# Performance work log

Measured on AMD Instinct MI355X. Metric: run time of the kernel, lower is better.

Reference implementation:

```python
import jax, jax.numpy as jnp
import numpy as np

B, N, E, D, F_IN, EDGE_DIM, VN = 128, 500, 1048576, 128, 5, 2, 10
NEG_FEAT = 0.01   # torch F.leaky_relu default
NEG_ATT = 0.2     # GAT attention slope


def _gat_layer(h_in, src, dst, edge_attr, W, b, a_src, a_dst, a_edge, We, n_nodes):
    # Edge-feature GAT conv: per-edge attention over (src, dst, edge) then
    # softmax-normalized scatter-aggregate onto destination nodes.
    h = h_in @ W                                  # [N, d]
    e = edge_attr @ We                            # [E, d] projected edge features
    logits = jax.nn.leaky_relu((h @ a_src)[src] + (h @ a_dst)[dst] + e @ a_edge,
                               negative_slope=NEG_ATT)    # [E]
    # segment softmax over incoming edges of each dst node
    m = jax.ops.segment_max(logits, dst, num_segments=n_nodes)
    ex = jnp.exp(logits - m[dst])
    denom = jax.ops.segment_sum(ex, dst, num_segments=n_nodes)
    alpha = ex / (denom[dst] + 1e-16)             # [E]
    msg = h[src] + e                              # [E, d]
    out = jax.ops.segment_sum(alpha[:, None] * msg, dst, num_segments=n_nodes)
    return out + b


def setup_inputs() -> dict:
    key = jax.random.key(0)
    ks = jax.random.split(key, 20)
    s = 0.05
    return {
        'x': jax.random.normal(ks[0], (B * N, F_IN), jnp.float32),
        'edge_index': jax.random.randint(ks[1], (2, E), 0, B * N, jnp.int64 if jax.config.jax_enable_x64 else jnp.int32).astype(jnp.int32),
        'edge_attr': jax.random.uniform(ks[2], (E, EDGE_DIM), jnp.float32),
        'curr_v_node_id': jax.random.randint(ks[3], (B,), 0, VN).astype(jnp.int32),
        'v_graph_embedding': jax.random.normal(ks[4], (B, D), jnp.float32),
        'v_node_dense_embeddings': jax.random.normal(ks[5], (B, VN, D), jnp.float32),
        'p_W': jax.random.normal(ks[6], (F_IN, D), jnp.float32) * s,
        'p_b': jnp.zeros((D,), jnp.float32),
        'Ws': jax.random.normal(ks[7], (4, D, D), jnp.float32) * s,
        'bs': jnp.zeros((4, D), jnp.float32),
        'a_srcs': jax.random.normal(ks[8], (4, D), jnp.float32) * s,
        'a_dsts': jax.random.normal(ks[9], (4, D), jnp.float32) * s,
        'a_edges': jax.random.normal(ks[10], (4, D), jnp.float32) * s,
        'Wes': jax.random.normal(ks[11], (4, EDGE_DIM, D), jnp.float32) * s,
        'W5': jax.random.normal(ks[12], (D, 1), jnp.float32) * s,
        'b5': jnp.zeros((1,), jnp.float32),
        'a_src5': jax.random.normal(ks[13], (1,), jnp.float32) * s,
        'a_dst5': jax.random.normal(ks[14], (1,), jnp.float32) * s,
        'a_edge5': jax.random.normal(ks[15], (1,), jnp.float32) * s,
        'We5': jax.random.normal(ks[16], (EDGE_DIM, 1), jnp.float32) * s,
    }


def reference(x, edge_index, edge_attr, curr_v_node_id, v_graph_embedding,
              v_node_dense_embeddings, p_W, p_b, Ws, bs, a_srcs, a_dsts,
              a_edges, Wes, W5, b5, a_src5, a_dst5, a_edge5, We5):
    n_nodes = x.shape[0]
    src, dst = edge_index[0], edge_index[1]
    # gather current v-node embedding: [B, D]
    curr_emb = v_node_dense_embeddings[jnp.arange(B), curr_v_node_id]
    # linear + leaky_relu then broadcast-add of graph/node context
    h = jax.nn.leaky_relu(x @ p_W + p_b, negative_slope=NEG_FEAT)  # [B*N, D]
    h = h.reshape(B, N, D) + v_graph_embedding[:, None, :] + curr_emb[:, None, :]
    h = h.reshape(B * N, D)
    # 4 hidden edge-feature GAT layers (128 -> 128) with leaky_relu
    for l in range(4):
        h = _gat_layer(h, src, dst, edge_attr, Ws[l], bs[l], a_srcs[l],
                       a_dsts[l], a_edges[l], Wes[l], n_nodes)
        h = jax.nn.leaky_relu(h, negative_slope=NEG_FEAT)
    # output layer (128 -> 1), no activation
    h = _gat_layer(h, src, dst, edge_attr, W5, b5, a_src5, a_dst5, a_edge5,
                   We5, n_nodes)                    # [B*N, 1]
    return h.reshape(B, N)
```

## Files before the change

kernel.cpp:

```cpp
#include <hip/hip_runtime.h>
#include <hip/hip_bf16.h>

#define BB   128
#define NN   500
#define NV   64000
#define EE   1048576
#define DD   128
#define FIN  5
#define VNN  10
#define NBUK 250
#define BCAP 8192

typedef unsigned int   uint32;
typedef unsigned short u16b;
typedef __attribute__((ext_vector_type(8))) short short8;
typedef __attribute__((ext_vector_type(4))) float float4v;

#define P_ASRC  0
#define P_ADST  512
#define P_WE    1024
#define P_BIAS  2048
#define P_W5    2560
#define P_CVEC  2688
#define P_SC5   2700
#define P_TOT   2816

static __device__ __forceinline__ float bf2f(__hip_bfloat16 v) { return __bfloat162float(v); }
static __device__ __forceinline__ float lo2f(uint32 u) { return __uint_as_float(u << 16); }
static __device__ __forceinline__ float hi2f(uint32 u) { return __uint_as_float(u & 0xFFFF0000u); }
static __device__ __forceinline__ uint32 f2bf_bits(float f) {
    uint32 u = __float_as_uint(f);
    return (u + 0x7FFFu + ((u >> 16) & 1u)) >> 16;
}
static __device__ __forceinline__ uint32 pack2(float a, float b) {
    return (f2bf_bits(a) & 0xFFFFu) | (f2bf_bits(b) << 16);
}
static __device__ __forceinline__ float ldf(const void* p, int i, int flag) {
    return flag ? ((const float*)p)[i] : bf2f(((const __hip_bfloat16*)p)[i]);
}

__global__ void sniff_kernel(const unsigned short* __restrict__ p16, int* __restrict__ FLAG) {
    __shared__ int sHigh, sZero;
    if (threadIdx.x == 0) { sHigh = 0; sZero = 0; }
    __syncthreads();
    unsigned short v = p16[2 * threadIdx.x];
    if (v >= 0x8000u) atomicOr(&sHigh, 1);
    if (v == 0)       atomicAdd(&sZero, 1);
    __syncthreads();
    if (threadIdx.x == 0) FLAG[0] = (sHigh || sZero >= 128) ? 1 : 0;
}

__global__ void zero_out_kernel(void* __restrict__ out, const int* __restrict__ FLAG, float tag) {
    int i = blockIdx.x * blockDim.x + threadIdx.x;
    if (i >= NV) return;
    float v = (i == 0) ? tag : 0.f;
    if (FLAG[0]) ((float*)out)[i] = v;
    else         ((u16b*)out)[i] = (u16b)f2bf_bits(v);
}

__global__ void prep_kernel(const void* __restrict__ Wes, const void* __restrict__ aeg,
                            const void* __restrict__ We5, const void* __restrict__ ae5,
                            const void* __restrict__ asr, const void* __restrict__ ads,
                            const void* __restrict__ bs, const void* __restrict__ W5,
                            const void* __restrict__ b5, const void* __restrict__ as5,
                            const void* __restrict__ ad5, const int* __restrict__ FLAG,
                            float* __restrict__ PAR) {
    const int flag = FLAG[0];
    if (blockIdx.x == 0) {
        for (int i = threadIdx.x; i < 512; i += 256) PAR[P_ASRC + i] = ldf(asr, i, flag);
    } else if (blockIdx.x == 1) {
        for (int i = threadIdx.x; i < 512; i += 256) PAR[P_ADST + i] = ldf(ads, i, flag);
    } else if (blockIdx.x == 2) {
        for (int i = threadIdx.x; i < 1024; i += 256) PAR[P_WE + i] = ldf(Wes, i, flag);
    } else if (blockIdx.x == 3) {
        for (int i = threadIdx.x; i < 512; i += 256) PAR[P_BIAS + i] = ldf(bs, i, flag);
    } else if (blockIdx.x == 4) {
        int tid = threadIdx.x;
        if (tid < 128) {
            PAR[P_W5 + tid] = ldf(W5, tid, flag);
        } else if (tid < 136) {
            int l = (tid - 128) >> 1, r = (tid - 128) & 1;
            float s = 0.f;
            for (int ch = 0; ch < DD; ++ch)
                s += ldf(Wes, l * 256 + r * DD + ch, flag) * ldf(aeg, l * DD + ch, flag);
            PAR[P_CVEC + l * 2 + r] = s;
        } else if (tid == 136) {
            float ae = ldf(ae5, 0, flag);
            float w0 = ldf(We5, 0, flag), w1 = ldf(We5, 1, flag);
            PAR[P_CVEC + 8] = w0 * ae; PAR[P_CVEC + 9] = w1 * ae;
            PAR[P_CVEC + 10] = w0;     PAR[P_CVEC + 11] = w1;
            PAR[P_SC5 + 0] = ldf(b5, 0, flag);
            PAR[P_SC5 + 1] = ldf(as5, 0, flag);
            PAR[P_SC5 + 2] = ldf(ad5, 0, flag);
        }
    }
}

__global__ __launch_bounds__(256) void prepack_kernel(const void* __restrict__ Ws,
                                                      const int* __restrict__ FLAG,
                                                      u16b* __restrict__ WB) {
    const int flag = FLAG[0];
    int t = blockIdx.x * 256 + threadIdx.x;
    int lane = t & 63;
    int frag = t >> 6;
    int nchunk = frag & 7, kblk = (frag >> 3) & 3, l = frag >> 5;
    int n = nchunk * 16 + (lane & 15);
    int kbase = kblk * 32 + (lane >> 4) * 8;
#pragma unroll
    for (int j = 0; j < 8; ++j) {
        int idx = l * 16384 + (kbase + j) * 128 + n;
        u16b bits = flag ? (u16b)f2bf_bits(((const float*)Ws)[idx])
                         : ((const u16b*)Ws)[idx];
        WB[(size_t)t * 8 + j] = bits;
    }
}

__global__ __launch_bounds__(256) void proj_kernel(
        const void* __restrict__ x, const void* __restrict__ pW,
        const void* __restrict__ pb, const int* __restrict__ curr,
        const void* __restrict__ vge, const void* __restrict__ vnd,
        const int* __restrict__ FLAG, uint32* __restrict__ H) {
    const int flag = FLAG[0];
    const int n = blockIdx.x * 4 + (threadIdx.x >> 6);
    const int lane = threadIdx.x & 63;
    const int b = n / NN;
    int cv = curr[b]; if ((unsigned)cv >= VNN) cv = 0;
    float xv[FIN];
#pragma unroll
    for (int k = 0; k < FIN; ++k) xv[k] = ldf(x, n * FIN + k, flag);
    const int ch = lane * 2;
    float s0 = ldf(pb, ch, flag), s1 = ldf(pb, ch + 1, flag);
#pragma unroll
    for (int k = 0; k < FIN; ++k) {
        s0 = fmaf(xv[k], ldf(pW, k * DD + ch, flag), s0);
        s1 = fmaf(xv[k], ldf(pW, k * DD + ch + 1, flag), s1);
    }
    s0 = (s0 > 0.f) ? s0 : 0.01f * s0;
    s1 = (s1 > 0.f) ? s1 : 0.01f * s1;
    s0 += ldf(vge, b * DD + ch, flag) + ldf(vnd, (b * VNN + cv) * DD + ch, flag);
    s1 += ldf(vge, b * DD + ch + 1, flag) + ldf(vnd, (b * VNN + cv) * DD + ch + 1, flag);
    H[(size_t)n * 64 + lane] = pack2(s0, s1);
}

__global__ void init_kernel(int* __restrict__ gcur, int* __restrict__ counts) {
    int t = blockIdx.x * 256 + threadIdx.x;
    if (t < NBUK) gcur[t] = t * BCAP;
    if (t < 512) counts[NV + t] = 0;
}

__global__ __launch_bounds__(256) void bucketize_kernel(
        const int* __restrict__ src, const int* __restrict__ dst,
        const void* __restrict__ eaP, const int* __restrict__ FLAG,
        int* __restrict__ gcur, uint32* __restrict__ bukx, uint32* __restrict__ buky) {
    __shared__ int cnt[256];
    __shared__ int cur[256];
    const int flag = FLAG[0];
    const int t = threadIdx.x;
    const int e0 = blockIdx.x * 4096;
    cnt[t] = 0;
    __syncthreads();
    int d[16];
#pragma unroll
    for (int i = 0; i < 16; ++i) {
        d[i] = dst[e0 + i * 256 + t];
        if ((unsigned)d[i] >= NV) d[i] = -1;
        if (d[i] >= 0) atomicAdd(&cnt[d[i] >> 8], 1);
    }
    __syncthreads();
    if (t < NBUK) {
        int c = cnt[t];
        cur[t] = c ? atomicAdd(&gcur[t], c) : 0;
    }
    __syncthreads();
#pragma unroll
    for (int i = 0; i < 16; ++i) {
        if (d[i] < 0) continue;
        int e = e0 + i * 256 + t;
        int b = d[i] >> 8;
        int s = src[e];
        if ((unsigned)s >= NV) s = 0;
        uint32 eb;
        if (flag) { float2 v = ((const float2*)eaP)[e]; eb = pack2(v.x, v.y); }
        else      eb = ((const uint32*)eaP)[e];
        int p = atomicAdd(&cur[b], 1);
        if (p < (b + 1) * BCAP) {
            bukx[p] = (uint32)((s & 0xFFFF) | ((d[i] & 255) << 16));
            buky[p] = eb;
        }
    }
}

__global__ __launch_bounds__(256) void bcount_kernel(
        const uint32* __restrict__ bukx, const int* __restrict__ gcur,
        int* __restrict__ counts) {
    __shared__ int c[256];
    const int b = blockIdx.x, t = threadIdx.x;
    c[t] = 0;
    __syncthreads();
    const int base = b * BCAP;
    int cnt = gcur[b] - base;
    if (cnt > BCAP) cnt = BCAP;
    for (int i = t; i < cnt; i += 256)
        atomicAdd(&c[(bukx[base + i] >> 16) & 255], 1);
    __syncthreads();
    counts[b * 256 + t] = c[t];
}

__global__ __launch_bounds__(256) void scan1_kernel(const int* __restrict__ counts,
                                                    int* __restrict__ row_ptr,
                                                    int* __restrict__ partials) {
    __shared__ int sdata[256];
    int tid = threadIdx.x;
    int4 v = ((const int4*)counts)[blockIdx.x * 256 + tid];
    int sum = v.x + v.y + v.z + v.w;
    sdata[tid] = sum;
    __syncthreads();
    int acc = sum;
    for (int off = 1; off < 256; off <<= 1) {
        int t = (tid >= off) ? sdata[tid - off] : 0;
        __syncthreads();
        acc += t;
        sdata[tid] = acc;
        __syncthreads();
    }
    int excl = acc - sum;
    int base = blockIdx.x * 1024 + tid * 4;
    int run = excl;
    if (base + 0 <= NV) row_ptr[base + 0] = run; run += v.x;
    if (base + 1 <= NV) row_ptr[base + 1] = run; run += v.y;
    if (base + 2 <= NV) row_ptr[base + 2] = run; run += v.z;
    if (base + 3 <= NV) row_ptr[base + 3] = run;
    if (tid == 255) partials[blockIdx.x] = acc;
}

__global__ __launch_bounds__(64) void scan2_kernel(const int* __restrict__ partials,
                                                   int* __restrict__ boff, int nb) {
    int lane = threadIdx.x;
    int v = (lane < nb) ? partials[lane] : 0;
    int orig = v;
#pragma unroll
    for (int off = 1; off < 64; off <<= 1) {
        int t = __shfl_up(v, off, 64);
        if (lane >= off) v += t;
    }
    boff[lane] = v - orig;
}

__global__ __launch_bounds__(256) void scan3_kernel(int* __restrict__ row_ptr,
                                                    const int* __restrict__ boff) {
    int add = boff[blockIdx.x];
    int base = blockIdx.x * 1024 + threadIdx.x * 4;
#pragma unroll
    for (int j = 0; j < 4; ++j) {
        int i = base + j;
        if (i <= NV) row_ptr[i] += add;
    }
}

__global__ __launch_bounds__(256) void bscatter_kernel(
        const uint32* __restrict__ bukx, const uint32* __restrict__ buky,
        const int* __restrict__ gcur, const int* __restrict__ row_ptr,
        int* __restrict__ csr_src, uint32* __restrict__ csr_ea) {
    __shared__ int cur[256];
    const int b = blockIdx.x, t = threadIdx.x;
    cur[t] = row_ptr[b * 256 + t];
    __syncthreads();
    const int base = b * BCAP;
    int cnt = gcur[b] - base;
    if (cnt > BCAP) cnt = BCAP;
    for (int i = t; i < cnt; i += 256) {
        uint32 x = bukx[base + i];
        uint32 y = buky[base + i];
        int p = atomicAdd(&cur[(x >> 16) & 255], 1);
        csr_src[p] = (int)(x & 0xFFFFu);
        csr_ea[p] = y;
    }
}

__global__ __launch_bounds__(256) void gemm_kernel(
        const uint32* __restrict__ Hu, const u16b* __restrict__ WBl,
        const float* __restrict__ PARl, uint32* __restrict__ HWu,
        float* __restrict__ ssrc, float* __restrict__ sdst) {
    __shared__ float hs[64 * 129];
    __shared__ float pp[512];
    const int tid = threadIdx.x;
    const int lane = tid & 63;
    const int wave = tid >> 6;
    const int quad = lane >> 4;
    const int n0 = blockIdx.x * 64;
    const int m = n0 + wave * 16 + (lane & 15);

    const u16b* hrow = (const u16b*)Hu + (size_t)m * 128;
    short8 a0 = *(const short8*)(hrow + 0  + quad * 8);
    short8 a1 = *(const short8*)(hrow + 32 + quad * 8);
    short8 a2 = *(const short8*)(hrow + 64 + quad * 8);
    short8 a3 = *(const short8*)(hrow + 96 + quad * 8);

#pragma unroll
    for (int nt = 0; nt < 8; ++nt) {
        const u16b* bbase = WBl + ((size_t)nt * 512 + lane * 8);
        short8 b0 = *(const short8*)(bbase + 0 * 4096);
        short8 b1 = *(const short8*)(bbase + 1 * 4096);
        short8 b2 = *(const short8*)(bbase + 2 * 4096);
        short8 b3 = *(const short8*)(bbase + 3 * 4096);
        float4v acc = {0.f, 0.f, 0.f, 0.f};
        acc = __builtin_amdgcn_mfma_f32_16x16x32_bf16(a0, b0, acc, 0, 0, 0);
        acc = __builtin_amdgcn_mfma_f32_16x16x32_bf16(a1, b1, acc, 0, 0, 0);
        acc = __builtin_amdgcn_mfma_f32_16x16x32_bf16(a2, b2, acc, 0, 0, 0);
        acc = __builtin_amdgcn_mfma_f32_16x16x32_bf16(a3, b3, acc, 0, 0, 0);
#pragma unroll
        for (int r = 0; r < 4; ++r)
            hs[(wave * 16 + quad * 4 + r) * 129 + nt * 16 + (lane & 15)] = acc[r];
    }
    __syncthreads();

    {
        const int mn = tid & 63, cg = tid >> 6;
        const float* Asr = PARl + P_ASRC;
        const float* Ads = PARl + P_ADST;
        const float* row = hs + mn * 129 + cg * 32;
        float ps = 0.f, pd = 0.f;
#pragma unroll
        for (int j = 0; j < 32; ++j) {
            float v = row[j];
            ps = fmaf(v, Asr[cg * 32 + j], ps);
            pd = fmaf(v, Ads[cg * 32 + j], pd);
        }
        pp[tid] = ps; pp[256 + tid] = pd;
    }
    __syncthreads();
    if (tid < 64) {
        ssrc[n0 + tid] = pp[tid] + pp[64 + tid] + pp[128 + tid] + pp[192 + tid];
        sdst[n0 + tid] = pp[256 + tid] + pp[320 + tid] + pp[384 + tid] + pp[448 + tid];
    }

#pragma unroll
    for (int i = 0; i < 4; ++i) {
        int flat = i * 2048 + tid * 8;
        int n = flat >> 7, c = flat & 127;
        const float* p = hs + n * 129 + c;
        uint4 v;
        v.x = pack2(p[0], p[1]); v.y = pack2(p[2], p[3]);
        v.z = pack2(p[4], p[5]); v.w = pack2(p[6], p[7]);
        *(uint4*)(HWu + (size_t)(n0 + n) * 64 + c / 2) = v;
    }
}

__global__ __launch_bounds__(256) void agg_kernel(
        const uint32* __restrict__ HWu, const float* __restrict__ ssrc,
        const float* __restrict__ sdst, const int* __restrict__ csr_src,
        const uint32* __restrict__ csr_ea, const int* __restrict__ row_ptr,
        const float* __restrict__ PAR, int layer, uint32* __restrict__ HoutU,
        float* __restrict__ hw5out, int wantw5) {
    __shared__ float exs[4][64];
    const int lane = threadIdx.x & 63;
    const int wid = threadIdx.x >> 6;
    const int n = blockIdx.x * 4 + wid;
    const int begin = __builtin_amdgcn_readfirstlane(row_ptr[n]);
    const int deg   = __builtin_amdgcn_readfirstlane(row_ptr[n + 1]) - begin;
    const float c0 = PAR[P_CVEC + 2 * layer], c1 = PAR[P_CVEC + 2 * layer + 1];
    const float sd = sdst[n];

    int   sv = 0;
    uint32 eb = 0;
    if (lane < deg) {
        sv = csr_src[begin + lane];
        eb = csr_ea[begin + lane];
    }
    const float ssv = ssrc[sv];

    const int dmain = (deg < 64) ? deg : 64;
    const int npad  = (dmain + 15) & ~15;

    uint32 hA[16], hB[16];
#pragma unroll
    for (int q = 0; q < 16; ++q) {
        int s = __builtin_amdgcn_readlane(sv, q);
        hA[q] = HWu[(s << 6) + lane];
    }
    if (npad > 16) {
#pragma unroll
        for (int q = 0; q < 16; ++q) {
            int s = __builtin_amdgcn_readlane(sv, 16 + q);
            hB[q] = HWu[(s << 6) + lane];
        }
    }

    float ex = 0.f;
    if (lane < deg) {
        float L = fmaf(hi2f(eb), c1, fmaf(lo2f(eb), c0, ssv + sd));
        L = (L > 0.f) ? L : 0.2f * L;
        ex = __expf(fminf(L, 60.f));
    }
    exs[wid][lane] = ex;

    float acc0 = 0.f, acc1 = 0.f;
    const float* wp = &exs[wid][0];
#pragma unroll
    for (int q0 = 0; q0 < 16; q0 += 4) {
        float4 w4 = *(const float4*)(wp + q0);
        acc0 = fmaf(w4.x, lo2f(hA[q0 + 0]), acc0); acc1 = fmaf(w4.x, hi2f(hA[q0 + 0]), acc1);
        acc0 = fmaf(w4.y, lo2f(hA[q0 + 1]), acc0); acc1 = fmaf(w4.y, hi2f(hA[q0 + 1]), acc1);
        acc0 = fmaf(w4.z, lo2f(hA[q0 + 2]), acc0); acc1 = fmaf(w4.z, hi2f(hA[q0 + 2]), acc1);
        acc0 = fmaf(w4.w, lo2f(hA[q0 + 3]), acc0); acc1 = fmaf(w4.w, hi2f(hA[q0 + 3]), acc1);
    }
    if (npad > 16) {
#pragma unroll
        for (int q0 = 16; q0 < 32; q0 += 4) {
            float4 w4 = *(const float4*)(wp + q0);
            acc0 = fmaf(w4.x, lo2f(hB[q0 - 16]), acc0); acc1 = fmaf(w4.x, hi2f(hB[q0 - 16]), acc1);
            acc0 = fmaf(w4.y, lo2f(hB[q0 - 15]), acc0); acc1 = fmaf(w4.y, hi2f(hB[q0 - 15]), acc1);
            acc0 = fmaf(w4.z, lo2f(hB[q0 - 14]), acc0); acc1 = fmaf(w4.z, hi2f(hB[q0 - 14]), acc1);
            acc0 = fmaf(w4.w, lo2f(hB[q0 - 13]), acc0); acc1 = fmaf(w4.w, hi2f(hB[q0 - 13]), acc1);
        }
    }
    for (int j = 32; j < dmain; ++j) {
        int s = __builtin_amdgcn_readlane(sv, j);
        float w = wp[j];
        uint32 hb = HWu[(s << 6) + lane];
        acc0 = fmaf(w, lo2f(hb), acc0);
        acc1 = fmaf(w, hi2f(hb), acc1);
    }

    float dsum = ex, sx = ex * lo2f(eb), sy = ex * hi2f(eb);
    for (int j0 = 64; j0 < deg; j0 += 64) {
        int j = j0 + lane;
        if (j < deg) {
            int s2 = csr_src[begin + j];
            uint32 e2 = csr_ea[begin + j];
            float L2 = fmaf(hi2f(e2), c1, fmaf(lo2f(e2), c0, ssrc[s2] + sd));
            L2 = (L2 > 0.f) ? L2 : 0.2f * L2;
            float x2 = __expf(fminf(L2, 60.f));
            dsum += x2; sx = fmaf(x2, lo2f(e2), sx); sy = fmaf(x2, hi2f(e2), sy);
        }
    }
#pragma unroll
    for (int o = 32; o; o >>= 1) {
        dsum += __shfl_xor(dsum, o, 64);
        sx   += __shfl_xor(sx, o, 64);
        sy   += __shfl_xor(sy, o, 64);
    }

    for (int jj = 64; jj < deg; ++jj) {
        int s = csr_src[begin + jj];
        uint32 e2 = csr_ea[begin + jj];
        float L2 = fmaf(hi2f(e2), c1, fmaf(lo2f(e2), c0, ssrc[s] + sd));
        L2 = (L2 > 0.f) ? L2 : 0.2f * L2;
        float x2 = __expf(fminf(L2, 60.f));
        uint32 hb = HWu[(size_t)s * 64 + lane];
        acc0 = fmaf(x2, lo2f(hb), acc0);
        acc1 = fmaf(x2, hi2f(hb), acc1);
    }

    const int ch = lane * 2;
    const float* WEl = PAR + P_WE + layer * 256;
    const float inv = __builtin_amdgcn_rcpf(dsum + 1e-16f);
    const float* Bl = PAR + P_BIAS + layer * DD;
    float t0 = fmaf(sy, WEl[DD + ch],     fmaf(sx, WEl[ch],     acc0));
    float t1 = fmaf(sy, WEl[DD + ch + 1], fmaf(sx, WEl[ch + 1], acc1));
    float o0 = fmaf(t0, inv, Bl[ch]);
    float o1 = fmaf(t1, inv, Bl[ch + 1]);
    o0 = (o0 > 0.f) ? o0 : 0.01f * o0;
    o1 = (o1 > 0.f) ? o1 : 0.01f * o1;
    HoutU[(size_t)n * 64 + lane] = pack2(o0, o1);

    if (wantw5) {
        float p = o0 * PAR[P_W5 + ch] + o1 * PAR[P_W5 + ch + 1];
#pragma unroll
        for (int o = 32; o; o >>= 1) p += __shfl_xor(p, o, 64);
        if (lane == 0) hw5out[n] = p;
    }
}

__global__ __launch_bounds__(256) void final_kernel(
        const float* __restrict__ hw5, const int* __restrict__ csr_src,
        const uint32* __restrict__ csr_ea, const int* __restrict__ row_ptr,
        const float* __restrict__ PAR, const int* __restrict__ FLAG,
        void* __restrict__ out) {
    const int flag = FLAG[0];
    int lane = threadIdx.x & 63;
    int n = blockIdx.x * 4 + (threadIdx.x >> 6);
    int begin = __builtin_amdgcn_readfirstlane(row_ptr[n]);
    int deg   = __builtin_amdgcn_readfirstlane(row_ptr[n + 1]) - begin;
    float c50 = PAR[P_CVEC + 8], c51 = PAR[P_CVEC + 9];
    float ce0 = PAR[P_CVEC + 10], ce1 = PAR[P_CVEC + 11];
    float b5v = PAR[P_SC5], a5s = PAR[P_SC5 + 1];
    float hd = PAR[P_SC5 + 2] * hw5[n];

    float dsum = 0.f, msum = 0.f;
    for (int j0 = 0; j0 < deg; j0 += 64) {
        int j = j0 + lane;
        if (j < deg) {
            int s = csr_src[begin + j];
            uint32 eb = csr_ea[begin + j];
            float hs5 = hw5[s];
            float L = fmaf(hi2f(eb), c51, fmaf(lo2f(eb), c50, fmaf(a5s, hs5, hd)));
            L = (L > 0.f) ? L : 0.2f * L;
            float ex = __expf(fminf(L, 60.f));
            dsum += ex;
            msum = fmaf(ex, hs5 + fmaf(hi2f(eb), ce1, lo2f(eb) * ce0), msum);
        }
    }
#pragma unroll
    for (int o = 32; o; o >>= 1) {
        dsum += __shfl_xor(dsum, o, 64);
        msum += __shfl_xor(msum, o, 64);
    }
    if (lane == 0) {
        float r = msum * __builtin_amdgcn_rcpf(dsum + 1e-16f) + b5v;
        if (flag) ((float*)out)[n] = r;
        else      ((u16b*)out)[n] = (u16b)f2bf_bits(r);
    }
}

extern "C" void kernel_launch(void* const* d_in, const int* in_sizes, int n_in,
                              void* d_out, int out_size, void* d_ws, size_t ws_size,
                              hipStream_t stream) {
    const void* x   = d_in[0];
    const int*  ei  = (const int*)d_in[1];
    const void* ea  = d_in[2];
    const int*  cur = (const int*)d_in[3];
    const void* vge = d_in[4];
    const void* vnd = d_in[5];
    const void* pW  = d_in[6];
    const void* pb  = d_in[7];
    const void* Ws  = d_in[8];
    const void* bs  = d_in[9];
    const void* asr = d_in[10];
    const void* ads = d_in[11];
    const void* aeg = d_in[12];
    const void* Wes = d_in[13];
    const void* W5  = d_in[14];
    const void* b5  = d_in[15];
    const void* as5 = d_in[16];
    const void* ad5 = d_in[17];
    const void* ae5 = d_in[18];
    const void* We5 = d_in[19];
    (void)in_sizes; (void)n_in; (void)out_size;

    const int* e_src = ei;
    const int* e_dst = ei + EE;

    size_t off = 0;
    char* base = (char*)d_ws;
    auto carve = [&](size_t bytes) {
        void* p = base + off;
        off += (bytes + 255) & ~(size_t)255;
        return p;
    };
    int*    FLAG   = (int*)carve(256);
    float*  PAR    = (float*)carve((size_t)P_TOT * 4);
    u16b*   WB     = (u16b*)carve(4 * DD * DD * 2);
    uint32* H0     = (uint32*)carve((size_t)NV * DD * 2);
    uint32* H1     = (uint32*)carve((size_t)NV * DD * 2);
    float*  SS     = (float*)carve(NV * 4);
    float*  SD     = (float*)carve(NV * 4);
    float*  HW5v   = (float*)carve(NV * 4);
    int*    COUNTS = (int*)carve(65536 * 4);
    int*    ROWPTR = (int*)carve(65536 * 4);
    int*    GCUR   = (int*)carve(256 * 4);
    int*    PART   = (int*)carve(256 * 4);
    int*    BOFF   = (int*)carve(256 * 4);
    int*    CSRS   = (int*)carve((size_t)EE * 4);
    uint32* CSREA  = (uint32*)carve((size_t)EE * 4);
    size_t need = off;

    uint32* BUKX = H1;
    uint32* BUKY = H1 + (size_t)NBUK * BCAP;

    sniff_kernel<<<1, 256, 0, stream>>>((const unsigned short*)ea, FLAG);

    if (need > ws_size) {
        zero_out_kernel<<<(NV + 255) / 256, 256, 0, stream>>>(
            d_out, FLAG, (float)(ws_size >> 20));
        return;
    }

    prep_kernel<<<5, 256, 0, stream>>>(Wes, aeg, We5, ae5, asr, ads, bs,
                                       W5, b5, as5, ad5, FLAG, PAR);
    prepack_kernel<<<32, 256, 0, stream>>>(Ws, FLAG, WB);
    proj_kernel<<<NV / 4, 256, 0, stream>>>(x, pW, pb, cur, vge, vnd, FLAG, H0);

    init_kernel<<<2, 256, 0, stream>>>(GCUR, COUNTS);
    bucketize_kernel<<<EE / 4096, 256, 0, stream>>>(e_src, e_dst, ea, FLAG,
                                                    GCUR, BUKX, BUKY);
    bcount_kernel<<<NBUK, 256, 0, stream>>>(BUKX, GCUR, COUNTS);
    scan1_kernel<<<63, 256, 0, stream>>>(COUNTS, ROWPTR, PART);
    scan2_kernel<<<1, 64, 0, stream>>>(PART, BOFF, 63);
    scan3_kernel<<<63, 256, 0, stream>>>(ROWPTR, BOFF);
    bscatter_kernel<<<NBUK, 256, 0, stream>>>(BUKX, BUKY, GCUR, ROWPTR,
                                              CSRS, CSREA);

    for (int l = 0; l < 4; ++l) {
        gemm_kernel<<<NV / 64, 256, 0, stream>>>(
            H0, WB + (size_t)l * 16384, PAR + l * DD, H1, SS, SD);
        agg_kernel<<<NV / 4, 256, 0, stream>>>(
            H1, SS, SD, CSRS, CSREA, ROWPTR, PAR, l, H0, HW5v, (l == 3) ? 1 : 0);
    }

    final_kernel<<<NV / 4, 256, 0, stream>>>(HW5v, CSRS, CSREA, ROWPTR, PAR,
                                             FLAG, d_out);
}
```

Before: 420.5 us.

## Interleave CSR arrays, fuse attention dot into GEMM epilogue, use packed float2 math

Merges the separate CSR source-index and edge-attribute arrays into one interleaved uint2 array, so each edge needs a single 8-byte load in aggregation and the final layer. The GEMM now computes the src/dst attention scores straight from the MFMA accumulators with interleaved a_src/a_dst vectors and shuffle reductions. This removes the shared-memory reduction pass and one barrier. The aggregation math is rewritten with float2 vector FMAs and 64-bit shuffles so the compiler can emit packed FP32 instructions. The cost is extra shuffles in the GEMM and a new block in the parameter prep kernel.

```diff
diff --git a/kernel.cpp b/kernel.cpp
--- a/kernel.cpp
+++ b/kernel.cpp
@@ -15,6 +15,7 @@
 typedef unsigned short u16b;
 typedef __attribute__((ext_vector_type(8))) short short8;
 typedef __attribute__((ext_vector_type(4))) float float4v;
+typedef __attribute__((ext_vector_type(2))) float float2v;
 
 #define P_ASRC  0
 #define P_ADST  512
@@ -23,7 +24,8 @@
 #define P_W5    2560
 #define P_CVEC  2688
 #define P_SC5   2700
-#define P_TOT   2816
+#define P_ASD   2816
+#define P_TOT   3840
 
 static __device__ __forceinline__ float bf2f(__hip_bfloat16 v) { return __bfloat162float(v); }
 static __device__ __forceinline__ float lo2f(uint32 u) { return __uint_as_float(u << 16); }
@@ -34,6 +36,38 @@
 }
 static __device__ __forceinline__ uint32 pack2(float a, float b) {
     return (f2bf_bits(a) & 0xFFFFu) | (f2bf_bits(b) << 16);
+}
+static __device__ __forceinline__ float2v unp2(uint32 u) {
+    float2v r; r.x = lo2f(u); r.y = hi2f(u); return r;
+}
+static __device__ __forceinline__ float2v fma2(float2v a, float2v b, float2v c) {
+#if __has_builtin(__builtin_elementwise_fma)
+    return __builtin_elementwise_fma(a, b, c);
+#else
+    float2v r; r.x = fmaf(a.x, b.x, c.x); r.y = fmaf(a.y, b.y, c.y); return r;
+#endif
+}
+static __device__ __forceinline__ float2v fma2s(float2v a, float w, float2v c) {
+    float2v ww = {w, w};
+    return fma2(a, ww, c);
+}
+static __device__ __forceinline__ float2v shfl_xor2(float2v v, int o) {
+    double d; __builtin_memcpy(&d, &v, 8);
+    d = __shfl_xor(d, o, 64);
+    float2v r; __builtin_memcpy(&r, &d, 8);
+    return r;
+}
+static __device__ __forceinline__ float2v lrelu2(float2v x, float slope) {
+    float2v z = {0.f, 0.f};
+#if __has_builtin(__builtin_elementwise_max)
+    float2v p = __builtin_elementwise_max(x, z);
+    float2v q = __builtin_elementwise_min(x, z);
+#else
+    float2v p; p.x = fmaxf(x.x, 0.f); p.y = fmaxf(x.y, 0.f);
+    float2v q; q.x = fminf(x.x, 0.f); q.y = fminf(x.y, 0.f);
+#endif
+    float2v s = {slope, slope};
+    return fma2(q, s, p);
 }
 static __device__ __forceinline__ float ldf(const void* p, int i, int flag) {
     return flag ? ((const float*)p)[i] : bf2f(((const __hip_bfloat16*)p)[i]);
@@ -93,6 +127,12 @@
             PAR[P_SC5 + 1] = ldf(as5, 0, flag);
             PAR[P_SC5 + 2] = ldf(ad5, 0, flag);
         }
+    } else if (blockIdx.x == 5) {
+        for (int i = threadIdx.x; i < 512; i += 256) {
+            int l = i >> 7, c = i & 127;
+            PAR[P_ASD + l * 256 + c * 2]     = ldf(asr, l * DD + c, flag);
+            PAR[P_ASD + l * 256 + c * 2 + 1] = ldf(ads, l * DD + c, flag);
+        }
     }
 }
 
@@ -260,7 +300,7 @@
 __global__ __launch_bounds__(256) void bscatter_kernel(
         const uint32* __restrict__ bukx, const uint32* __restrict__ buky,
         const int* __restrict__ gcur, const int* __restrict__ row_ptr,
-        int* __restrict__ csr_src, uint32* __restrict__ csr_ea) {
+        uint2* __restrict__ csr2) {
     __shared__ int cur[256];
     const int b = blockIdx.x, t = threadIdx.x;
     cur[t] = row_ptr[b * 256 + t];
@@ -272,17 +312,15 @@
         uint32 x = bukx[base + i];
         uint32 y = buky[base + i];
         int p = atomicAdd(&cur[(x >> 16) & 255], 1);
-        csr_src[p] = (int)(x & 0xFFFFu);
-        csr_ea[p] = y;
+        csr2[p] = make_uint2(x & 0xFFFFu, y);
     }
 }
 
 __global__ __launch_bounds__(256) void gemm_kernel(
         const uint32* __restrict__ Hu, const u16b* __restrict__ WBl,
-        const float* __restrict__ PARl, uint32* __restrict__ HWu,
+        const float* __restrict__ ASDl, uint32* __restrict__ HWu,
         float* __restrict__ ssrc, float* __restrict__ sdst) {
     __shared__ float hs[64 * 129];
-    __shared__ float pp[512];
     const int tid = threadIdx.x;
     const int lane = tid & 63;
     const int wave = tid >> 6;
@@ -295,6 +333,11 @@
     short8 a1 = *(const short8*)(hrow + 32 + quad * 8);
     short8 a2 = *(const short8*)(hrow + 64 + quad * 8);
     short8 a3 = *(const short8*)(hrow + 96 + quad * 8);
+
+    const float2v* asd = (const float2v*)ASDl;
+    float2v psd[4];
+#pragma unroll
+    for (int r = 0; r < 4; ++r) { psd[r].x = 0.f; psd[r].y = 0.f; }
 
 #pragma unroll
     for (int nt = 0; nt < 8; ++nt) {
@@ -308,31 +351,30 @@
         acc = __builtin_amdgcn_mfma_f32_16x16x32_bf16(a1, b1, acc, 0, 0, 0);
         acc = __builtin_amdgcn_mfma_f32_16x16x32_bf16(a2, b2, acc, 0, 0, 0);
         acc = __builtin_amdgcn_mfma_f32_16x16x32_bf16(a3, b3, acc, 0, 0, 0);
-#pragma unroll
-        for (int r = 0; r < 4; ++r)
+        float2v av = asd[nt * 16 + (lane & 15)];
+#pragma unroll
+        for (int r = 0; r < 4; ++r) {
             hs[(wave * 16 + quad * 4 + r) * 129 + nt * 16 + (lane & 15)] = acc[r];
-    }
-    __syncthreads();
-
-    {
-        const int mn = tid & 63, cg = tid >> 6;
-        const float* Asr = PARl + P_ASRC;
-        const float* Ads = PARl + P_ADST;
-        const float* row = hs + mn * 129 + cg * 32;
-        float ps = 0.f, pd = 0.f;
-#pragma unroll
-        for (int j = 0; j < 32; ++j) {
-            float v = row[j];
-            ps = fmaf(v, Asr[cg * 32 + j], ps);
-            pd = fmaf(v, Ads[cg * 32 + j], pd);
-        }
-        pp[tid] = ps; pp[256 + tid] = pd;
-    }
-    __syncthreads();
-    if (tid < 64) {
-        ssrc[n0 + tid] = pp[tid] + pp[64 + tid] + pp[128 + tid] + pp[192 + tid];
-        sdst[n0 + tid] = pp[256 + tid] + pp[320 + tid] + pp[384 + tid] + pp[448 + tid];
-    }
+            psd[r] = fma2s(av, acc[r], psd[r]);
+        }
+    }
+#pragma unroll
+    for (int r = 0; r < 4; ++r) {
+#pragma unroll
+        for (int o = 1; o < 16; o <<= 1) {
+            float2v other = shfl_xor2(psd[r], o);
+            psd[r].x += other.x; psd[r].y += other.y;
+        }
+    }
+    if ((lane & 15) == 0) {
+#pragma unroll
+        for (int r = 0; r < 4; ++r) {
+            int row = n0 + wave * 16 + quad * 4 + r;
+            ssrc[row] = psd[r].x;
+            sdst[row] = psd[r].y;
+        }
+    }
+    __syncthreads();
 
 #pragma unroll
     for (int i = 0; i < 4; ++i) {
@@ -348,9 +390,9 @@
 
 __global__ __launch_bounds__(256) void agg_kernel(
         const uint32* __restrict__ HWu, const float* __restrict__ ssrc,
-        const float* __restrict__ sdst, const int* __restrict__ csr_src,
-        const uint32* __restrict__ csr_ea, const int* __restrict__ row_ptr,
-        const float* __restrict__ PAR, int layer, uint32* __restrict__ HoutU,
+        const float* __restrict__ sdst, const uint2* __restrict__ csr2,
+        const int* __restrict__ row_ptr, const float* __restrict__ PAR,
+        int layer, uint32* __restrict__ HoutU,
         float* __restrict__ hw5out, int wantw5) {
     __shared__ float exs[4][64];
     const int lane = threadIdx.x & 63;
@@ -364,8 +406,9 @@
     int   sv = 0;
     uint32 eb = 0;
     if (lane < deg) {
-        sv = csr_src[begin + lane];
-        eb = csr_ea[begin + lane];
+        uint2 se = csr2[begin + lane];
+        sv = (int)se.x;
+        eb = se.y;
     }
     const float ssv = ssrc[sv];
 
@@ -394,78 +437,75 @@
     }
     exs[wid][lane] = ex;
 
-    float acc0 = 0.f, acc1 = 0.f;
+    float2v acc2 = {0.f, 0.f};
     const float* wp = &exs[wid][0];
 #pragma unroll
     for (int q0 = 0; q0 < 16; q0 += 4) {
         float4 w4 = *(const float4*)(wp + q0);
-        acc0 = fmaf(w4.x, lo2f(hA[q0 + 0]), acc0); acc1 = fmaf(w4.x, hi2f(hA[q0 + 0]), acc1);
-        acc0 = fmaf(w4.y, lo2f(hA[q0 + 1]), acc0); acc1 = fmaf(w4.y, hi2f(hA[q0 + 1]), acc1);
-        acc0 = fmaf(w4.z, lo2f(hA[q0 + 2]), acc0); acc1 = fmaf(w4.z, hi2f(hA[q0 + 2]), acc1);
-        acc0 = fmaf(w4.w, lo2f(hA[q0 + 3]), acc0); acc1 = fmaf(w4.w, hi2f(hA[q0 + 3]), acc1);
+        acc2 = fma2s(unp2(hA[q0 + 0]), w4.x, acc2);
+        acc2 = fma2s(unp2(hA[q0 + 1]), w4.y, acc2);
+        acc2 = fma2s(unp2(hA[q0 + 2]), w4.z, acc2);
+        acc2 = fma2s(unp2(hA[q0 + 3]), w4.w, acc2);
     }
     if (npad > 16) {
 #pragma unroll
         for (int q0 = 16; q0 < 32; q0 += 4) {
             float4 w4 = *(const float4*)(wp + q0);
-            acc0 = fmaf(w4.x, lo2f(hB[q0 - 16]), acc0); acc1 = fmaf(w4.x, hi2f(hB[q0 - 16]), acc1);
-            acc0 = fmaf(w4.y, lo2f(hB[q0 - 15]), acc0); acc1 = fmaf(w4.y, hi2f(hB[q0 - 15]), acc1);
-            acc0 = fmaf(w4.z, lo2f(hB[q0 - 14]), acc0); acc1 = fmaf(w4.z, hi2f(hB[q0 - 14]), acc1);
-            acc0 = fmaf(w4.w, lo2f(hB[q0 - 13]), acc0); acc1 = fmaf(w4.w, hi2f(hB[q0 - 13]), acc1);
+            acc2 = fma2s(unp2(hB[q0 - 16]), w4.x, acc2);
+            acc2 = fma2s(unp2(hB[q0 - 15]), w4.y, acc2);
+            acc2 = fma2s(unp2(hB[q0 - 14]), w4.z, acc2);
+            acc2 = fma2s(unp2(hB[q0 - 13]), w4.w, acc2);
         }
     }
     for (int j = 32; j < dmain; ++j) {
         int s = __builtin_amdgcn_readlane(sv, j);
         float w = wp[j];
-        uint32 hb = HWu[(s << 6) + lane];
-        acc0 = fmaf(w, lo2f(hb), acc0);
-        acc1 = fmaf(w, hi2f(hb), acc1);
-    }
-
-    float dsum = ex, sx = ex * lo2f(eb), sy = ex * hi2f(eb);
+        acc2 = fma2s(unp2(HWu[(s << 6) + lane]), w, acc2);
+    }
+
+    float dsum = ex;
+    float2v sxy = unp2(eb);
+    sxy.x *= ex; sxy.y *= ex;
     for (int j0 = 64; j0 < deg; j0 += 64) {
         int j = j0 + lane;
         if (j < deg) {
-            int s2 = csr_src[begin + j];
-            uint32 e2 = csr_ea[begin + j];
-            float L2 = fmaf(hi2f(e2), c1, fmaf(lo2f(e2), c0, ssrc[s2] + sd));
+            uint2 se2 = csr2[begin + j];
+            float L2 = fmaf(hi2f(se2.y), c1, fmaf(lo2f(se2.y), c0, ssrc[se2.x] + sd));
             L2 = (L2 > 0.f) ? L2 : 0.2f * L2;
             float x2 = __expf(fminf(L2, 60.f));
-            dsum += x2; sx = fmaf(x2, lo2f(e2), sx); sy = fmaf(x2, hi2f(e2), sy);
+            dsum += x2;
+            sxy = fma2s(unp2(se2.y), x2, sxy);
         }
     }
 #pragma unroll
     for (int o = 32; o; o >>= 1) {
         dsum += __shfl_xor(dsum, o, 64);
-        sx   += __shfl_xor(sx, o, 64);
-        sy   += __shfl_xor(sy, o, 64);
+        float2v other = shfl_xor2(sxy, o);
+        sxy.x += other.x; sxy.y += other.y;
     }
 
     for (int jj = 64; jj < deg; ++jj) {
-        int s = csr_src[begin + jj];
-        uint32 e2 = csr_ea[begin + jj];
-        float L2 = fmaf(hi2f(e2), c1, fmaf(lo2f(e2), c0, ssrc[s] + sd));
+        uint2 se2 = csr2[begin + jj];
+        float L2 = fmaf(hi2f(se2.y), c1, fmaf(lo2f(se2.y), c0, ssrc[se2.x] + sd));
         L2 = (L2 > 0.f) ? L2 : 0.2f * L2;
         float x2 = __expf(fminf(L2, 60.f));
-        uint32 hb = HWu[(size_t)s * 64 + lane];
-        acc0 = fmaf(x2, lo2f(hb), acc0);
-        acc1 = fmaf(x2, hi2f(hb), acc1);
+        acc2 = fma2s(unp2(HWu[(size_t)se2.x * 64 + lane]), x2, acc2);
     }
 
     const int ch = lane * 2;
     const float* WEl = PAR + P_WE + layer * 256;
     const float inv = __builtin_amdgcn_rcpf(dsum + 1e-16f);
     const float* Bl = PAR + P_BIAS + layer * DD;
-    float t0 = fmaf(sy, WEl[DD + ch],     fmaf(sx, WEl[ch],     acc0));
-    float t1 = fmaf(sy, WEl[DD + ch + 1], fmaf(sx, WEl[ch + 1], acc1));
-    float o0 = fmaf(t0, inv, Bl[ch]);
-    float o1 = fmaf(t1, inv, Bl[ch + 1]);
-    o0 = (o0 > 0.f) ? o0 : 0.01f * o0;
-    o1 = (o1 > 0.f) ? o1 : 0.01f * o1;
-    HoutU[(size_t)n * 64 + lane] = pack2(o0, o1);
+    float2v we0 = *(const float2v*)(WEl + ch);
+    float2v we1 = *(const float2v*)(WEl + DD + ch);
+    float2v bl  = *(const float2v*)(Bl + ch);
+    float2v t2 = fma2s(we1, sxy.y, fma2s(we0, sxy.x, acc2));
+    float2v o2 = fma2s(t2, inv, bl);
+    o2 = lrelu2(o2, 0.01f);
+    HoutU[(size_t)n * 64 + lane] = pack2(o2.x, o2.y);
 
     if (wantw5) {
-        float p = o0 * PAR[P_W5 + ch] + o1 * PAR[P_W5 + ch + 1];
+        float p = o2.x * PAR[P_W5 + ch] + o2.y * PAR[P_W5 + ch + 1];
 #pragma unroll
         for (int o = 32; o; o >>= 1) p += __shfl_xor(p, o, 64);
         if (lane == 0) hw5out[n] = p;
@@ -473,10 +513,9 @@
 }
 
 __global__ __launch_bounds__(256) void final_kernel(
-        const float* __restrict__ hw5, const int* __restrict__ csr_src,
-        const uint32* __restrict__ csr_ea, const int* __restrict__ row_ptr,
-        const float* __restrict__ PAR, const int* __restrict__ FLAG,
-        void* __restrict__ out) {
+        const float* __restrict__ hw5, const uint2* __restrict__ csr2,
+        const int* __restrict__ row_ptr, const float* __restrict__ PAR,
+        const int* __restrict__ FLAG, void* __restrict__ out) {
     const int flag = FLAG[0];
     int lane = threadIdx.x & 63;
     int n = blockIdx.x * 4 + (threadIdx.x >> 6);
@@ -491,14 +530,13 @@
     for (int j0 = 0; j0 < deg; j0 += 64) {
         int j = j0 + lane;
         if (j < deg) {
-            int s = csr_src[begin + j];
-            uint32 eb = csr_ea[begin + j];
-            float hs5 = hw5[s];
-            float L = fmaf(hi2f(eb), c51, fmaf(lo2f(eb), c50, fmaf(a5s, hs5, hd)));
+            uint2 se = csr2[begin + j];
+            float hs5 = hw5[se.x];
+            float L = fmaf(hi2f(se.y), c51, fmaf(lo2f(se.y), c50, fmaf(a5s, hs5, hd)));
             L = (L > 0.f) ? L : 0.2f * L;
             float ex = __expf(fminf(L, 60.f));
             dsum += ex;
-            msum = fmaf(ex, hs5 + fmaf(hi2f(eb), ce1, lo2f(eb) * ce0), msum);
+            msum = fmaf(ex, hs5 + fmaf(hi2f(se.y), ce1, lo2f(se.y) * ce0), msum);
         }
     }
 #pragma unroll
@@ -561,8 +599,7 @@
     int*    GCUR   = (int*)carve(256 * 4);
     int*    PART   = (int*)carve(256 * 4);
     int*    BOFF   = (int*)carve(256 * 4);
-    int*    CSRS   = (int*)carve((size_t)EE * 4);
-    uint32* CSREA  = (uint32*)carve((size_t)EE * 4);
+    uint2*  CSR2   = (uint2*)carve((size_t)EE * 8);
     size_t need = off;
 
     uint32* BUKX = H1;
@@ -576,7 +613,7 @@
         return;
     }
 
-    prep_kernel<<<5, 256, 0, stream>>>(Wes, aeg, We5, ae5, asr, ads, bs,
+    prep_kernel<<<6, 256, 0, stream>>>(Wes, aeg, We5, ae5, asr, ads, bs,
                                        W5, b5, as5, ad5, FLAG, PAR);
     prepack_kernel<<<32, 256, 0, stream>>>(Ws, FLAG, WB);
     proj_kernel<<<NV / 4, 256, 0, stream>>>(x, pW, pb, cur, vge, vnd, FLAG, H0);
@@ -588,16 +625,15 @@
     scan1_kernel<<<63, 256, 0, stream>>>(COUNTS, ROWPTR, PART);
     scan2_kernel<<<1, 64, 0, stream>>>(PART, BOFF, 63);
     scan3_kernel<<<63, 256, 0, stream>>>(ROWPTR, BOFF);
-    bscatter_kernel<<<NBUK, 256, 0, stream>>>(BUKX, BUKY, GCUR, ROWPTR,
-                                              CSRS, CSREA);
+    bscatter_kernel<<<NBUK, 256, 0, stream>>>(BUKX, BUKY, GCUR, ROWPTR, CSR2);
 
     for (int l = 0; l < 4; ++l) {
         gemm_kernel<<<NV / 64, 256, 0, stream>>>(
-            H0, WB + (size_t)l * 16384, PAR + l * DD, H1, SS, SD);
+            H0, WB + (size_t)l * 16384, PAR + P_ASD + l * 256, H1, SS, SD);
         agg_kernel<<<NV / 4, 256, 0, stream>>>(
-            H1, SS, SD, CSRS, CSREA, ROWPTR, PAR, l, H0, HW5v, (l == 3) ? 1 : 0);
-    }
-
-    final_kernel<<<NV / 4, 256, 0, stream>>>(HW5v, CSRS, CSREA, ROWPTR, PAR,
+            H1, SS, SD, CSR2, ROWPTR, PAR, l, H0, HW5v, (l == 3) ? 1 : 0);
+    }
+
+    final_kernel<<<NV / 4, 256, 0, stream>>>(HW5v, CSR2, ROWPTR, PAR,
                                              FLAG, d_out);
 }
```

New measurement: 421.1 us. Within noise of the previous version (+0.1%).
